# Kernel optimization log

Measured on AMD Instinct MI355X. Metric: run time of the kernel, lower is better.

The kernel has to match this reference:

```python
import jax, jax.numpy as jnp
import numpy as np

K = 20
EPS = 1e-5


def _bn(h, g, b, axes):
    m = jnp.mean(h, axes, keepdims=True)
    v = jnp.var(h, axes, keepdims=True)
    return (h - m) * jax.lax.rsqrt(v + EPS) * g + b


def _edge_feat(h):
    # h: [B,N,D] -> edge features [B,N,K,2D] = concat(central, neighbor-central)
    sq = jnp.sum(h * h, -1)
    # negative squared pairwise distance (larger = closer)
    adj = 2.0 * jnp.einsum('bnd,bmd->bnm', h, h) - sq[:, :, None] - sq[:, None, :]
    idx = jax.lax.top_k(adj, K)[1]  # [B,N,K] nearest (incl. self)
    nbr = jax.vmap(lambda hb, ib: hb[ib])(h, idx)  # [B,N,K,D]
    ctr = jnp.broadcast_to(h[:, :, None, :], nbr.shape)
    return jnp.concatenate([ctr, nbr - ctr], -1)


def _edge_layer(h, W, b, g, be):
    # 1x1 conv over edge features, relu THEN batchnorm (matches torch: bn(relu(conv))), max over K
    ef = _edge_feat(h)
    z = jax.nn.relu(jnp.einsum('bnkc,oc->bnko', ef, W) + b)
    z = _bn(z, g, be, (0, 1, 2))
    return jnp.max(z, axis=2)  # [B,N,O]


def _c1d(h, W, b):
    return jnp.einsum('bcl,oc->bol', h, W) + b[None, :, None]


def _bnc(h, g, b):
    m = jnp.mean(h, (0, 2), keepdims=True)
    v = jnp.var(h, (0, 2), keepdims=True)
    return (h - m) * jax.lax.rsqrt(v + EPS) * g[None, :, None] + b[None, :, None]


def _forward(x, rand_grid, W1, b1, g1, be1, W2, b2, g2, be2, W3, b3, g3, be3,
             W4, b4, g4, be4, W5, b5, g5, be5, lW, lb, lg, lbe,
             dW1, db1, dg1, dbe1, dW2, db2, dg2, dbe2, dW3, db3, dg3, dbe3, dW4, db4):
    pts = jnp.transpose(x, (0, 2, 1))  # [B,N,3]
    x1 = _edge_layer(pts, W1, b1, g1, be1)   # [B,N,64]
    x2 = _edge_layer(x1, W2, b2, g2, be2)    # [B,N,64]
    x3 = _edge_layer(x2, W3, b3, g3, be3)    # [B,N,64]
    x4 = _edge_layer(x3, W4, b4, g4, be4)    # [B,N,128]
    cat = jnp.concatenate([x1, x2, x3, x4], -1)  # [B,N,320]
    z = jax.nn.relu(jnp.einsum('bnc,oc->bno', cat, W5) + b5)
    z = _bn(z, g5, be5, (0, 1))
    glob = jnp.max(z, axis=1)  # [B,1024]
    lat = glob @ lW.T + lb
    lat = jax.nn.relu(_bn(lat, lg, lbe, (0,)))  # [B,1024]
    B, C = lat.shape
    P = rand_grid.shape[2]
    y = jnp.concatenate([rand_grid, jnp.broadcast_to(lat[:, :, None], (B, C, P))], axis=1)  # [B,1026,P]
    h = jax.nn.relu(_bnc(_c1d(y, dW1, db1), dg1, dbe1))
    h = jax.nn.relu(_bnc(_c1d(h, dW2, db2), dg2, dbe2))
    h = jax.nn.relu(_bnc(_c1d(h, dW3, db3), dg3, dbe3))
    return jnp.tanh(_c1d(h, dW4, db4))  # [B,3,P]


def setup_inputs() -> dict:
    key = jax.random.key(0)
    ks = iter(jax.random.split(key, 64))
    B, N, BOT = 8, 2048, 1024
    D = BOT + 2  # 1026
    f32 = jnp.float32

    def w(o, c):
        return jax.random.normal(next(ks), (o, c), dtype=f32) * 0.05

    def bnp(c):
        return jnp.ones((c,), f32), jnp.zeros((c,), f32)

    inp = {
        'x': jax.random.normal(next(ks), (B, 3, N), dtype=f32),
        'rand_grid': jax.random.uniform(next(ks), (B, 2, N), dtype=f32),
    }
    enc = [(64, 6), (64, 128), (64, 128), (128, 128), (1024, 320)]
    for i, (o, c) in enumerate(enc, 1):
        inp[f'W{i}'] = w(o, c)
        inp[f'b{i}'] = jnp.zeros((o,), f32)
        inp[f'g{i}'], inp[f'be{i}'] = bnp(o)
    inp['lW'] = w(BOT, 1024)
    inp['lb'] = jnp.zeros((BOT,), f32)
    inp['lg'], inp['lbe'] = bnp(BOT)
    dec = [(D, D), (D // 2, D), (D // 4, D // 2), (3, D // 4)]
    for i, (o, c) in enumerate(dec, 1):
        inp[f'dW{i}'] = w(o, c)
        inp[f'db{i}'] = jnp.zeros((o,), f32)
        if i < 4:
            inp[f'dg{i}'], inp[f'dbe{i}'] = bnp(o)
    return inp


def reference(x, rand_grid, W1, b1, g1, be1, W2, b2, g2, be2, W3, b3, g3, be3,
              W4, b4, g4, be4, W5, b5, g5, be5, lW, lb, lg, lbe,
              dW1, db1, dg1, dbe1, dW2, db2, dg2, dbe2, dW3, db3, dg3, dbe3, dW4, db4):
    return _forward(x, rand_grid, W1, b1, g1, be1, W2, b2, g2, be2, W3, b3, g3, be3,
                    W4, b4, g4, be4, W5, b5, g5, be5, lW, lb, lg, lbe,
                    dW1, db1, dg1, dbe1, dW2, db2, dg2, dbe2, dW3, db3, dg3, dbe3, dW4, db4)
```

## Files before the change

### kernel.cpp

```cpp
#include <hip/hip_runtime.h>
#include <math.h>

constexpr int NB = 8;
constexpr int NN = 2048;
constexpr int NK = 20;
constexpr int NP = 2048;


__global__ void transpose_x_kernel(const float* __restrict__ x, float* __restrict__ pts) {
  int gid = blockIdx.x * 256 + threadIdx.x;
  if (gid >= NB * NN * 3) return;
  int c = gid % 3;
  int n = (gid / 3) % NN;
  int b = gid / (3 * NN);
  pts[gid] = x[(b * 3 + c) * NN + n];
}

__global__ void transpose_mat_ld(const float* __restrict__ src, float* __restrict__ dst, int R,
                                 int C, int ldd) {
  __shared__ float tile[32][33];
  int c0 = blockIdx.x * 32, r0 = blockIdx.y * 32;
  int tx = threadIdx.x & 31, ty = threadIdx.x >> 5;
  for (int i = ty; i < 32; i += 8) {
    int r = r0 + i, c = c0 + tx;
    tile[i][tx] = (r < R && c < C) ? src[(size_t)r * C + c] : 0.f;
  }
  __syncthreads();
  for (int i = ty; i < 32; i += 8) {
    int c = c0 + i, r = r0 + tx;
    if (r < R && c < C) dst[(size_t)c * ldd + r] = tile[tx][i];
  }
}

__global__ void knn3_fused_kernel(const float* __restrict__ pts, int* __restrict__ idx) {
  __shared__ float sm[3][NN];
  int t = threadIdx.x;
  int l = t & 63, w = t >> 6;
  int gb = blockIdx.x;
  int b = gb >> 9;
  int n0 = (gb & 511) * 4;
  const float* base = pts + (size_t)b * NN * 3;
  for (int e = t; e < NN * 3; e += 256) {
    int col = e / 3, d = e - col * 3;
    sm[d][col] = base[e];
  }
  __syncthreads();
  int n = n0 + w;
  float c0 = sm[0][n], c1 = sm[1][n], c2 = sm[2][n];
  float v[32];
#pragma unroll
  for (int j = 0; j < 32; j++) {
    int col = j * 64 + l;
    float d0 = c0 - sm[0][col];
    float d1 = c1 - sm[1][col];
    float d2 = c2 - sm[2][col];
    float acc = 0.f;
    acc = fmaf(d0, d0, acc);
    acc = fmaf(d1, d1, acc);
    acc = fmaf(d2, d2, acc);
    v[j] = -acc;
  }
  int mykm = 0;
  for (int k = 0; k < NK; k++) {
    float bv = v[0];
    int bj = 0;
#pragma unroll
    for (int j = 1; j < 32; j++) {
      if (v[j] > bv) { bv = v[j]; bj = j; }
    }
    int gm = bj * 64 + l;
#pragma unroll
    for (int off = 32; off; off >>= 1) {
      float ov = __shfl_xor(bv, off, 64);
      int om = __shfl_xor(gm, off, 64);
      if (ov > bv || (ov == bv && om < gm)) { bv = ov; gm = om; }
    }
    if (l == k) mykm = gm;
    int jb = gm >> 6, lb = gm & 63;
#pragma unroll
    for (int j = 0; j < 32; j++)
      if (j == jb && l == lb) v[j] = -3e38f;
  }
  if (l < NK) idx[((size_t)(b * NN + n)) * NK + l] = mykm;
}

__global__ __launch_bounds__(1024) void knn64_fused_kernel(const float* __restrict__ h, int ld,
                                                           int coff, int* __restrict__ idx) {
  __shared__ float sft[64][128];
  __shared__ float sctr[16][64];
  int t = threadIdx.x;
  int l = t & 63, w = t >> 6;
  int n0 = blockIdx.x * 16;
  int b = blockIdx.y;
  const float* rows = h + (size_t)b * NN * ld + coff;
  {
    int r = t >> 6, d = t & 63;
    sctr[r][d] = rows[(size_t)(n0 + r) * ld + d];
  }
  int col_l = t >> 3;
  int d0 = (t & 7) * 8;
  float v[32];
#pragma unroll
  for (int ct = 0; ct < 16; ct++) {
    __syncthreads();
    {
      const float* src = &rows[(size_t)(ct * 128 + col_l) * ld + d0];
      float4 f0 = *(const float4*)src;
      float4 f1 = *(const float4*)(src + 4);
      sft[d0 + 0][col_l] = f0.x;
      sft[d0 + 1][col_l] = f0.y;
      sft[d0 + 2][col_l] = f0.z;
      sft[d0 + 3][col_l] = f0.w;
      sft[d0 + 4][col_l] = f1.x;
      sft[d0 + 5][col_l] = f1.y;
      sft[d0 + 6][col_l] = f1.z;
      sft[d0 + 7][col_l] = f1.w;
    }
    __syncthreads();
    float a0 = 0.f, a1 = 0.f;
#pragma unroll 8
    for (int d = 0; d < 64; d++) {
      float cd = sctr[w][d];
      float2 f = *(const float2*)&sft[d][2 * l];
      float e0 = cd - f.x, e1 = cd - f.y;
      a0 = fmaf(e0, e0, a0);
      a1 = fmaf(e1, e1, a1);
    }
    v[2 * ct] = -a0;
    v[2 * ct + 1] = -a1;
  }
  int mykm = 0;
  for (int k = 0; k < NK; k++) {
    float bv = v[0];
    int bj = 0;
#pragma unroll
    for (int j = 1; j < 32; j++) {
      if (v[j] > bv) { bv = v[j]; bj = j; }
    }
    int gm = ((bj >> 1) << 7) + 2 * l + (bj & 1);
#pragma unroll
    for (int off = 32; off; off >>= 1) {
      float ov = __shfl_xor(bv, off, 64);
      int om = __shfl_xor(gm, off, 64);
      if (ov > bv || (ov == bv && om < gm)) { bv = ov; gm = om; }
    }
    if (l == k) mykm = gm;
    int rem = gm & 127;
    int jb = ((gm >> 7) << 1) + (rem & 1);
    int lb = rem >> 1;
#pragma unroll
    for (int j = 0; j < 32; j++)
      if (j == jb && l == lb) v[j] = -3e38f;
  }
  if (l < NK) idx[((size_t)(b * NN + n0 + w)) * NK + l] = mykm;
}

__global__ void weff_kernel(const float* __restrict__ W, int O, int D, float* __restrict__ Weff) {
  int i = blockIdx.x * 256 + threadIdx.x;
  if (i >= 2 * O * D) return;
  int o = i / D, d = i - o * D;
  float v;
  if (o < O) v = W[(size_t)o * 2 * D + d] - W[(size_t)o * 2 * D + D + d];
  else v = W[(size_t)(o - O) * 2 * D + D + d];
  Weff[i] = v;
}

template <int M2, int D>
__global__ __launch_bounds__(256, 4) void pgemm_kernel(const float* __restrict__ h, int ld,
                                                       int coff, const float* __restrict__ Weff,
                                                       const float* __restrict__ bias,
                                                       float* __restrict__ P) {
  constexpr int O = M2 / 2;
  constexpr int GRP = 256 / M2;
  constexpr int NR = 8 / GRP;
  __shared__ float sh[8][D == 3 ? 4 : 68];
  int t = threadIdx.x;
  int n0 = blockIdx.x * 8;
  const float* base = h + coff;
  if constexpr (D == 64) {
    if (t < 128) {
      int r = t >> 4, q = (t & 15) * 4;
      *(float4*)&sh[r][q] = *(const float4*)&base[(size_t)(n0 + r) * ld + q];
    }
  } else {
    if (t < 24) {
      int r = t / 3, c = t - r * 3;
      sh[r][c] = base[(size_t)(n0 + r) * ld + c];
    }
  }
  __syncthreads();
  int o = t % M2;
  int gi = t / M2;
  float acc[NR];
  float bz = (o < O) ? bias[o] : 0.f;
#pragma unroll
  for (int j = 0; j < NR; j++) acc[j] = bz;
  const float* wr = Weff + (size_t)o * D;
  if constexpr (D == 64) {
#pragma unroll
    for (int d4 = 0; d4 < 16; d4++) {
      float4 w4 = *(const float4*)&wr[d4 * 4];
#pragma unroll
      for (int j = 0; j < NR; j++) {
        float4 e4 = *(const float4*)&sh[gi * NR + j][d4 * 4];
        acc[j] = fmaf(w4.x, e4.x, acc[j]);
        acc[j] = fmaf(w4.y, e4.y, acc[j]);
        acc[j] = fmaf(w4.z, e4.z, acc[j]);
        acc[j] = fmaf(w4.w, e4.w, acc[j]);
      }
    }
  } else {
    float w0 = wr[0], w1 = wr[1], w2 = wr[2];
#pragma unroll
    for (int j = 0; j < NR; j++) {
      int r = gi * NR + j;
      acc[j] = fmaf(w0, sh[r][0], fmaf(w1, sh[r][1], fmaf(w2, sh[r][2], acc[j])));
    }
  }
#pragma unroll
  for (int j = 0; j < NR; j++)
    P[(size_t)(n0 + gi * NR + j) * M2 + o] = acc[j];
}

template <int O>
__global__ __launch_bounds__(256, 8) void combine_kernel(const float* __restrict__ P,
                                                         const int* __restrict__ idx,
                                                         float* __restrict__ zmax,
                                                         float* __restrict__ zmin,
                                                         float* __restrict__ psum,
                                                         float* __restrict__ psq) {
  constexpr int CPB = 256 / O;
  constexpr int M2 = 2 * O;
  __shared__ int sidx[CPB * NK];
  int t = threadIdx.x;
  int bn0 = blockIdx.x * CPB;
  if (t < CPB * NK) sidx[t] = idx[(size_t)bn0 * NK + t];
  __syncthreads();
  int g = t / O, o = t % O;
  int bn = bn0 + g;
  int b = bn >> 11;
  float p1 = P[(size_t)bn * M2 + o];
  const float* P2 = P + (size_t)b * NN * M2 + O + o;
  float s = 0.f, sq = 0.f, mx = -3e38f, mn = 3e38f;
#pragma unroll
  for (int k = 0; k < NK; k++) {
    int nb = sidx[g * NK + k];
    float z = fmaxf(p1 + P2[(size_t)nb * M2], 0.f);
    s += z;
    sq = fmaf(z, z, sq);
    mx = fmaxf(mx, z);
    mn = fminf(mn, z);
  }
  zmax[(size_t)bn * O + o] = mx;
  zmin[(size_t)bn * O + o] = mn;
  psum[(size_t)o * (NB * NN) + bn] = s;
  psq[(size_t)o * (NB * NN) + bn] = sq;
}

__global__ void edge_reduce_kernel(const float* __restrict__ psum, const float* __restrict__ psq,
                                   const float* __restrict__ g, const float* __restrict__ be,
                                   float* __restrict__ scale, float* __restrict__ shift,
                                   double inv_n) {
  int o = blockIdx.x, t = threadIdx.x;
  double s = 0.0, q = 0.0;
  const float* ps = psum + (size_t)o * (NB * NN);
  const float* pq = psq + (size_t)o * (NB * NN);
  for (int i = t; i < NB * NN; i += 256) { s += (double)ps[i]; q += (double)pq[i]; }
  __shared__ double rs[256], rq[256];
  rs[t] = s; rq[t] = q;
  __syncthreads();
  for (int st = 128; st; st >>= 1) {
    if (t < st) { rs[t] += rs[t + st]; rq[t] += rq[t + st]; }
    __syncthreads();
  }
  if (t == 0) {
    double mean = rs[0] * inv_n;
    double var = rq[0] * inv_n - mean * mean;
    double r = 1.0 / sqrt(var + 1e-5);
    double sc = (double)g[o] * r;
    scale[o] = (float)sc;
    shift[o] = (float)((double)be[o] - mean * sc);
  }
}

__global__ void edge_affine_kernel(const float* __restrict__ zmax, const float* __restrict__ zmin,
                                   const float* __restrict__ scale, const float* __restrict__ shift,
                                   float* __restrict__ cat, int O, int coff_out) {
  int gid = blockIdx.x * 256 + threadIdx.x;
  int o = gid % O;
  int bn = gid / O;
  float sc = scale[o];
  float v = (sc >= 0.f) ? zmax[gid] : zmin[gid];
  cat[(size_t)bn * 320 + coff_out + o] = fmaf(sc, v, shift[o]);
}

__global__ __launch_bounds__(256, 2) void gemm5_64_kernel(const float* __restrict__ cat,
                                                          const float* __restrict__ W5t,
                                                          const float* __restrict__ b5,
                                                          float* __restrict__ z5) {
  __shared__ float sA[32][64];
  __shared__ float sB[32][128];
  int t = threadIdx.x;
  int r0 = blockIdx.x * 64, m0 = blockIdx.y * 128;
  int arow = t & 63, ach = (t >> 6) * 8;
  int blr = t >> 4, blc = (t & 15) * 8;
  int tx = t & 15, ty = t >> 4;
  float acc[4][8] = {};
  float rA[8], rB[16];

  auto gload = [&](int c0) {
    const float* pa = &cat[(size_t)(r0 + arow) * 320 + c0 + ach];
    float4 a0 = *(const float4*)pa;
    float4 a1 = *(const float4*)(pa + 4);
    rA[0] = a0.x; rA[1] = a0.y; rA[2] = a0.z; rA[3] = a0.w;
    rA[4] = a1.x; rA[5] = a1.y; rA[6] = a1.z; rA[7] = a1.w;
    const float* pb = &W5t[(size_t)(c0 + blr) * 1024 + m0 + blc];
    float4 b0 = *(const float4*)pb;
    float4 b1 = *(const float4*)(pb + 4);
    rB[0] = b0.x; rB[1] = b0.y; rB[2] = b0.z; rB[3] = b0.w;
    rB[4] = b1.x; rB[5] = b1.y; rB[6] = b1.z; rB[7] = b1.w;
    const float* pb2 = &W5t[(size_t)(c0 + 16 + blr) * 1024 + m0 + blc];
    float4 c4 = *(const float4*)pb2;
    float4 c5 = *(const float4*)(pb2 + 4);
    rB[8] = c4.x; rB[9] = c4.y; rB[10] = c4.z; rB[11] = c4.w;
    rB[12] = c5.x; rB[13] = c5.y; rB[14] = c5.z; rB[15] = c5.w;
  };
  auto ldswrite = [&]() {
#pragma unroll
    for (int j = 0; j < 8; j++) sA[ach + j][arow] = rA[j];
    float4 w0, w1;
    w0.x = rB[0]; w0.y = rB[1]; w0.z = rB[2]; w0.w = rB[3];
    w1.x = rB[4]; w1.y = rB[5]; w1.z = rB[6]; w1.w = rB[7];
    *(float4*)&sB[blr][blc] = w0;
    *(float4*)&sB[blr][blc + 4] = w1;
    w0.x = rB[8]; w0.y = rB[9]; w0.z = rB[10]; w0.w = rB[11];
    w1.x = rB[12]; w1.y = rB[13]; w1.z = rB[14]; w1.w = rB[15];
    *(float4*)&sB[16 + blr][blc] = w0;
    *(float4*)&sB[16 + blr][blc + 4] = w1;
  };

  gload(0);
  for (int kt = 0; kt < 10; kt++) {
    __syncthreads();
    ldswrite();
    __syncthreads();
    if (kt + 1 < 10) gload((kt + 1) * 32);
#pragma unroll
    for (int c = 0; c < 32; c++) {
      float4 a0 = *(const float4*)&sA[c][ty * 4];
      float4 b0 = *(const float4*)&sB[c][tx * 4];
      float4 b1 = *(const float4*)&sB[c][64 + tx * 4];
      float av[4] = {a0.x, a0.y, a0.z, a0.w};
      float bv[8] = {b0.x, b0.y, b0.z, b0.w, b1.x, b1.y, b1.z, b1.w};
#pragma unroll
      for (int i = 0; i < 4; i++)
#pragma unroll
        for (int j = 0; j < 8; j++) acc[i][j] = fmaf(av[i], bv[j], acc[i][j]);
    }
  }
  float bj[8];
#pragma unroll
  for (int j = 0; j < 8; j++)
    bj[j] = b5[m0 + (j < 4 ? tx * 4 + j : 64 + tx * 4 + (j - 4))];
#pragma unroll
  for (int i = 0; i < 4; i++) {
    int r = r0 + ty * 4 + i;
    float* dst = &z5[(size_t)r * 1024 + m0];
    float4 q0, q1;
    q0.x = fmaxf(acc[i][0] + bj[0], 0.f);
    q0.y = fmaxf(acc[i][1] + bj[1], 0.f);
    q0.z = fmaxf(acc[i][2] + bj[2], 0.f);
    q0.w = fmaxf(acc[i][3] + bj[3], 0.f);
    q1.x = fmaxf(acc[i][4] + bj[4], 0.f);
    q1.y = fmaxf(acc[i][5] + bj[5], 0.f);
    q1.z = fmaxf(acc[i][6] + bj[6], 0.f);
    q1.w = fmaxf(acc[i][7] + bj[7], 0.f);
    *(float4*)&dst[tx * 4] = q0;
    *(float4*)&dst[64 + tx * 4] = q1;
  }
}

__global__ void stats5_kernel(const float* __restrict__ z5, double* __restrict__ psum5,
                              double* __restrict__ psq5, float* __restrict__ pmax5,
                              float* __restrict__ pmin5) {
  int j = blockIdx.x, t = threadIdx.x;
  int row0 = j * 64;
  double s0 = 0, s1 = 0, s2 = 0, s3 = 0, q0 = 0, q1 = 0, q2 = 0, q3 = 0;
  float4 mx = {-3e38f, -3e38f, -3e38f, -3e38f}, mn = {3e38f, 3e38f, 3e38f, 3e38f};
  for (int r = 0; r < 64; r++) {
    float4 v = *(const float4*)&z5[(size_t)(row0 + r) * 1024 + t * 4];
    s0 += v.x; s1 += v.y; s2 += v.z; s3 += v.w;
    q0 += (double)v.x * v.x; q1 += (double)v.y * v.y;
    q2 += (double)v.z * v.z; q3 += (double)v.w * v.w;
    mx.x = fmaxf(mx.x, v.x); mx.y = fmaxf(mx.y, v.y); mx.z = fmaxf(mx.z, v.z); mx.w = fmaxf(mx.w, v.w);
    mn.x = fminf(mn.x, v.x); mn.y = fminf(mn.y, v.y); mn.z = fminf(mn.z, v.z); mn.w = fminf(mn.w, v.w);
  }
  size_t base = (size_t)j * 1024 + t * 4;
  psum5[base + 0] = s0; psum5[base + 1] = s1; psum5[base + 2] = s2; psum5[base + 3] = s3;
  psq5[base + 0] = q0; psq5[base + 1] = q1; psq5[base + 2] = q2; psq5[base + 3] = q3;
  *(float4*)&pmax5[base] = mx;
  *(float4*)&pmin5[base] = mn;
}

__global__ void reduce5_glob_kernel(const double* __restrict__ psum5, const double* __restrict__ psq5,
                                    const float* __restrict__ pmax5, const float* __restrict__ pmin5,
                                    const float* __restrict__ g5, const float* __restrict__ be5,
                                    float* __restrict__ glob) {
  int o = blockIdx.x * 256 + threadIdx.x;
  double s = 0.0, q = 0.0;
  for (int j = 0; j < 256; j++) {
    s += psum5[(size_t)j * 1024 + o];
    q += psq5[(size_t)j * 1024 + o];
  }
  double mean = s * (1.0 / 16384.0);
  double var = q * (1.0 / 16384.0) - mean * mean;
  double r = 1.0 / sqrt(var + 1e-5);
  double scd = (double)g5[o] * r;
  float sc = (float)scd;
  float sh = (float)((double)be5[o] - mean * scd);
  for (int b = 0; b < 8; b++) {
    float m;
    if (sc >= 0.f) {
      m = -3e38f;
      for (int jj = 0; jj < 32; jj++) m = fmaxf(m, pmax5[(size_t)(b * 32 + jj) * 1024 + o]);
    } else {
      m = 3e38f;
      for (int jj = 0; jj < 32; jj++) m = fminf(m, pmin5[(size_t)(b * 32 + jj) * 1024 + o]);
    }
    glob[b * 1024 + o] = fmaf(sc, m, sh);
  }
}

__global__ void fc_kernel(const float* __restrict__ in, const float* __restrict__ Wt, int ld,
                          int coff, const float* __restrict__ bias, float* __restrict__ out,
                          int Ci, int Co) {
  __shared__ float sin_[1024];
  __shared__ float red[8][32];
  int b = blockIdx.x, t = threadIdx.x;
  for (int e = t; e < Ci; e += 256) sin_[e] = in[(size_t)b * Ci + e];
  __syncthreads();
  int o = blockIdx.y * 32 + (t & 31);
  int cg = t >> 5;
  int cn = Ci / 8;
  float p = 0.f;
  if (o < Co) {
    for (int c = cg * cn; c < (cg + 1) * cn; c++)
      p = fmaf(Wt[(size_t)(c + coff) * ld + o], sin_[c], p);
  }
  red[cg][t & 31] = p;
  __syncthreads();
  if (cg == 0 && o < Co) {
    float s = red[0][t] + red[1][t] + red[2][t] + red[3][t] + red[4][t] + red[5][t] + red[6][t] +
              red[7][t];
    out[(size_t)b * Co + o] = s + bias[o];
  }
}

__global__ void lat_bn_kernel(const float* __restrict__ latp, const float* __restrict__ lg,
                              const float* __restrict__ lbe, float* __restrict__ lat) {
  int o = blockIdx.x * 256 + threadIdx.x;
  float v[8];
  double s = 0.0, q = 0.0;
  for (int b = 0; b < 8; b++) {
    v[b] = latp[b * 1024 + o];
    s += (double)v[b];
    q += (double)v[b] * (double)v[b];
  }
  double mean = s * 0.125;
  double var = q * 0.125 - mean * mean;
  double r = 1.0 / sqrt(var + 1e-5);
  double gd = (double)lg[o], bd = (double)lbe[o];
  for (int b = 0; b < 8; b++) {
    float z = (float)(((double)v[b] - mean) * r * gd + bd);
    lat[b * 1024 + o] = fmaxf(z, 0.f);
  }
}

__global__ void dec1_z_kernel(const float* __restrict__ rg, const float* __restrict__ dW1t,
                              const float* __restrict__ u, float* __restrict__ z1) {
  int bo = blockIdx.x;
  int b = bo / 1026;
  int o = bo - b * 1026;
  int t = threadIdx.x;
  float w0 = dW1t[o], w1 = dW1t[1026 + o], ub = u[bo];
  const float4* r0 = (const float4*)(rg + (size_t)b * 2 * NP);
  const float4* r1 = (const float4*)(rg + (size_t)b * 2 * NP + NP);
  float4* zr = (float4*)(z1 + (size_t)bo * NP);
  for (int i = t; i < NP / 4; i += 256) {
    float4 a = r0[i], c = r1[i], rr;
    rr.x = fmaf(w0, a.x, fmaf(w1, c.x, ub));
    rr.y = fmaf(w0, a.y, fmaf(w1, c.y, ub));
    rr.z = fmaf(w0, a.z, fmaf(w1, c.z, ub));
    rr.w = fmaf(w0, a.w, fmaf(w1, c.w, ub));
    zr[i] = rr;
  }
}

__global__ void dstats_kernel(const float* __restrict__ z, int C, const float* __restrict__ g,
                              const float* __restrict__ be, float* __restrict__ scale,
                              float* __restrict__ shift) {
  int o = blockIdx.x, t = threadIdx.x;
  double s = 0.0, q = 0.0;
  for (int b = 0; b < 8; b++) {
    const float4* row = (const float4*)(z + ((size_t)b * C + o) * NP);
    for (int i = t; i < NP / 4; i += 256) {
      float4 v = row[i];
      s += (double)v.x + (double)v.y + (double)v.z + (double)v.w;
      q += (double)v.x * v.x + (double)v.y * v.y + (double)v.z * v.z + (double)v.w * v.w;
    }
  }
  __shared__ double rs[256], rq[256];
  rs[t] = s; rq[t] = q;
  __syncthreads();
  for (int st = 128; st; st >>= 1) {
    if (t < st) { rs[t] += rs[t + st]; rq[t] += rq[t + st]; }
    __syncthreads();
  }
  if (t == 0) {
    double inv = 1.0 / (8.0 * NP);
    double mean = rs[0] * inv;
    double var = rq[0] * inv - mean * mean;
    double r = 1.0 / sqrt(var + 1e-5);
    double sc = (double)g[o] * r;
    scale[o] = (float)sc;
    shift[o] = (float)((double)be[o] - mean * sc);
  }
}

template <int NMT>
__global__ __launch_bounds__(256, 2) void dec_gemm64s_kernel(
    const float* __restrict__ zin, const float* __restrict__ Wt, int ldA,
    const float* __restrict__ bias, const float* __restrict__ scale,
    const float* __restrict__ shift, float* __restrict__ zout, int Ci, int Co) {
  __shared__ float sA[32][64];
  __shared__ float sB[32][128];
  int bid = blockIdx.x;
  int gl = bid & 7;
  int q = bid >> 3;
  int gh = q / NMT;
  int mt = q - gh * NMT;
  int g = gl + (gh << 3);
  int pt = g & 15;
  int b = g >> 4;
  int m0 = mt * 64, p0 = pt * 128;
  int t = threadIdx.x;
  int lr = t >> 4, lcA = (t & 15) * 4, lcB = (t & 15) * 8;
  int tx = t & 15, ty = t >> 4;
  int numK = (Ci + 31) >> 5;
  float acc[4][8] = {};
  float rA[8], rB[16];

  auto gloadhalf = [&](int c, float* ra, float* rb) {
#pragma unroll
    for (int j = 0; j < 4; j++) ra[j] = 0.f;
#pragma unroll
    for (int j = 0; j < 8; j++) rb[j] = 0.f;
    if (c < Ci) {
      int mb = m0 + lcA;
      if (mb + 4 <= Co) {
        float4 a0 = *(const float4*)&Wt[(size_t)c * ldA + mb];
        ra[0] = a0.x; ra[1] = a0.y; ra[2] = a0.z; ra[3] = a0.w;
      } else {
#pragma unroll
        for (int j = 0; j < 4; j++)
          if (mb + j < Co) ra[j] = Wt[(size_t)c * ldA + mb + j];
      }
      float sc = scale[c], sh = shift[c];
      const float* src = &zin[((size_t)b * Ci + c) * NP + p0 + lcB];
      float4 z0 = *(const float4*)src;
      float4 z1 = *(const float4*)(src + 4);
      rb[0] = fmaxf(fmaf(sc, z0.x, sh), 0.f);
      rb[1] = fmaxf(fmaf(sc, z0.y, sh), 0.f);
      rb[2] = fmaxf(fmaf(sc, z0.z, sh), 0.f);
      rb[3] = fmaxf(fmaf(sc, z0.w, sh), 0.f);
      rb[4] = fmaxf(fmaf(sc, z1.x, sh), 0.f);
      rb[5] = fmaxf(fmaf(sc, z1.y, sh), 0.f);
      rb[6] = fmaxf(fmaf(sc, z1.z, sh), 0.f);
      rb[7] = fmaxf(fmaf(sc, z1.w, sh), 0.f);
    }
  };
  auto gload = [&](int kt) {
    gloadhalf(kt * 32 + lr, rA, rB);
    gloadhalf(kt * 32 + 16 + lr, rA + 4, rB + 8);
  };
  auto ldswrite = [&]() {
    float4 v0;
    v0.x = rA[0]; v0.y = rA[1]; v0.z = rA[2]; v0.w = rA[3];
    *(float4*)&sA[lr][lcA] = v0;
    v0.x = rA[4]; v0.y = rA[5]; v0.z = rA[6]; v0.w = rA[7];
    *(float4*)&sA[16 + lr][lcA] = v0;
    float4 w0, w1;
    w0.x = rB[0]; w0.y = rB[1]; w0.z = rB[2]; w0.w = rB[3];
    w1.x = rB[4]; w1.y = rB[5]; w1.z = rB[6]; w1.w = rB[7];
    *(float4*)&sB[lr][lcB] = w0;
    *(float4*)&sB[lr][lcB + 4] = w1;
    w0.x = rB[8]; w0.y = rB[9]; w0.z = rB[10]; w0.w = rB[11];
    w1.x = rB[12]; w1.y = rB[13]; w1.z = rB[14]; w1.w = rB[15];
    *(float4*)&sB[16 + lr][lcB] = w0;
    *(float4*)&sB[16 + lr][lcB + 4] = w1;
  };

  gload(0);
  for (int kt = 0; kt < numK; kt++) {
    __syncthreads();
    ldswrite();
    __syncthreads();
    if (kt + 1 < numK) gload(kt + 1);
#pragma unroll
    for (int c = 0; c < 32; c++) {
      float4 a0 = *(const float4*)&sA[c][ty * 4];
      float4 b0 = *(const float4*)&sB[c][tx * 4];
      float4 b1 = *(const float4*)&sB[c][64 + tx * 4];
      float av[4] = {a0.x, a0.y, a0.z, a0.w};
      float bv[8] = {b0.x, b0.y, b0.z, b0.w, b1.x, b1.y, b1.z, b1.w};
#pragma unroll
      for (int i = 0; i < 4; i++)
#pragma unroll
        for (int j = 0; j < 8; j++) acc[i][j] = fmaf(av[i], bv[j], acc[i][j]);
    }
  }
#pragma unroll
  for (int i = 0; i < 4; i++) {
    int m = m0 + ty * 4 + i;
    if (m < Co) {
      float bv = bias[m];
      float* dst = &zout[((size_t)b * Co + m) * NP + p0];
      float4 q0, q1;
      q0.x = acc[i][0] + bv; q0.y = acc[i][1] + bv;
      q0.z = acc[i][2] + bv; q0.w = acc[i][3] + bv;
      q1.x = acc[i][4] + bv; q1.y = acc[i][5] + bv;
      q1.z = acc[i][6] + bv; q1.w = acc[i][7] + bv;
      *(float4*)&dst[tx * 4] = q0;
      *(float4*)&dst[64 + tx * 4] = q1;
    }
  }
}

__global__ void dec_final_kernel(const float* __restrict__ z3, const float* __restrict__ dW4,
                                 const float* __restrict__ db4, const float* __restrict__ scale,
                                 const float* __restrict__ shift, float* __restrict__ out) {
  __shared__ float w4[3 * 256];
  __shared__ float sc[256], sh[256];
  __shared__ float red[4][64][3];
  int b = blockIdx.x, pc = blockIdx.y, t = threadIdx.x;
  for (int e = t; e < 768; e += 256) w4[e] = dW4[e];
  sc[t] = scale[t];
  sh[t] = shift[t];
  __syncthreads();
  int tp = t & 63, tc = t >> 6;
  int p = pc * 64 + tp;
  float a0 = 0.f, a1 = 0.f, a2 = 0.f;
  for (int c = tc * 64; c < tc * 64 + 64; c++) {
    float hv = fmaxf(fmaf(sc[c], z3[((size_t)(b * 256 + c)) * NP + p], sh[c]), 0.f);
    a0 = fmaf(w4[c], hv, a0);
    a1 = fmaf(w4[256 + c], hv, a1);
    a2 = fmaf(w4[512 + c], hv, a2);
  }
  red[tc][tp][0] = a0;
  red[tc][tp][1] = a1;
  red[tc][tp][2] = a2;
  __syncthreads();
  if (tc == 0) {
    a0 = red[0][tp][0] + red[1][tp][0] + red[2][tp][0] + red[3][tp][0];
    a1 = red[0][tp][1] + red[1][tp][1] + red[2][tp][1] + red[3][tp][1];
    a2 = red[0][tp][2] + red[1][tp][2] + red[2][tp][2] + red[3][tp][2];
    out[((size_t)b * 3 + 0) * NP + p] = tanhf(a0 + db4[0]);
    out[((size_t)b * 3 + 1) * NP + p] = tanhf(a1 + db4[1]);
    out[((size_t)b * 3 + 2) * NP + p] = tanhf(a2 + db4[2]);
  }
}


extern "C" void kernel_launch(void* const* d_in, const int* in_sizes, int n_in, void* d_out,
                              int out_size, void* d_ws, size_t ws_size, hipStream_t stream) {
  const float* x = (const float*)d_in[0];
  const float* rg = (const float*)d_in[1];
  const float* W1 = (const float*)d_in[2];
  const float* b1 = (const float*)d_in[3];
  const float* g1 = (const float*)d_in[4];
  const float* be1 = (const float*)d_in[5];
  const float* W2 = (const float*)d_in[6];
  const float* b2 = (const float*)d_in[7];
  const float* g2 = (const float*)d_in[8];
  const float* be2 = (const float*)d_in[9];
  const float* W3 = (const float*)d_in[10];
  const float* b3 = (const float*)d_in[11];
  const float* g3 = (const float*)d_in[12];
  const float* be3 = (const float*)d_in[13];
  const float* W4 = (const float*)d_in[14];
  const float* b4 = (const float*)d_in[15];
  const float* g4 = (const float*)d_in[16];
  const float* be4 = (const float*)d_in[17];
  const float* W5 = (const float*)d_in[18];
  const float* b5 = (const float*)d_in[19];
  const float* g5 = (const float*)d_in[20];
  const float* be5 = (const float*)d_in[21];
  const float* lW = (const float*)d_in[22];
  const float* lb = (const float*)d_in[23];
  const float* lg = (const float*)d_in[24];
  const float* lbe = (const float*)d_in[25];
  const float* dW1 = (const float*)d_in[26];
  const float* db1 = (const float*)d_in[27];
  const float* dg1 = (const float*)d_in[28];
  const float* dbe1 = (const float*)d_in[29];
  const float* dW2 = (const float*)d_in[30];
  const float* db2 = (const float*)d_in[31];
  const float* dg2 = (const float*)d_in[32];
  const float* dbe2 = (const float*)d_in[33];
  const float* dW3 = (const float*)d_in[34];
  const float* db3 = (const float*)d_in[35];
  const float* dg3 = (const float*)d_in[36];
  const float* dbe3 = (const float*)d_in[37];
  const float* dW4 = (const float*)d_in[38];
  const float* db4 = (const float*)d_in[39];
  float* out = (float*)d_out;

  float* ws = (float*)d_ws;
  size_t off = 0;
  auto alloc = [&](size_t n) {
    size_t r = off;
    off += (n + 255) & ~(size_t)255;
    return r;
  };
  size_t f_pts = alloc((size_t)NB * NN * 3);
  size_t f_uA = alloc(13959168);
  size_t f_cat = f_uA;
  size_t f_idx = f_cat + 5242880;
  size_t f_zmax = f_idx + 327680;
  size_t f_zmin = f_zmax + 2097152;
  size_t f_psum = f_zmin + 2097152;
  size_t f_psq = f_psum + 2097152;
  size_t f_z2 = f_uA;
  size_t f_uB = alloc(16809984);
  size_t f_z5 = f_uB, f_z1 = f_uB;
  float* P = ws + f_uB;
  size_t f_uC = alloc(4194304);
  double* ps5_d = (double*)(ws + f_uC);
  double* pq5_d = ps5_d + 262144;
  size_t f_pM5 = f_uC + 2097152;
  size_t f_pm5 = f_pM5 + 262144;
  size_t f_z3 = f_uC;
  size_t f_weff = alloc(256 * 64);
  size_t f_W5t = alloc(320 * 1024);
  size_t f_lWt = alloc(1024 * 1024);
  size_t f_dW1t = alloc((size_t)1026 * 1026);
  size_t f_dW2t = alloc((size_t)1026 * 516);
  size_t f_dW3t = alloc(513 * 256);
  size_t f_scale = alloc(2048);
  size_t f_shift = alloc(2048);
  size_t f_glob = alloc(8 * 1024);
  size_t f_latp = alloc(8 * 1024);
  size_t f_lat = alloc(8 * 1024);
  size_t f_u = alloc(8 * 1026);
  (void)ws_size;
  (void)in_sizes;
  (void)n_in;
  (void)out_size;

  float* cat = ws + f_cat;
  int* idxp = (int*)(ws + f_idx);
  float* zmax = ws + f_zmax;
  float* zmin = ws + f_zmin;
  float* psumf = ws + f_psum;
  float* psqf = ws + f_psq;
  float* weff = ws + f_weff;
  float* scale = ws + f_scale;
  float* shift = ws + f_shift;
  const double invn_e = 1.0 / (double)(NB * NN * NK);

  transpose_x_kernel<<<192, 256, 0, stream>>>(x, ws + f_pts);
  transpose_mat_ld<<<dim3(10, 32), 256, 0, stream>>>(W5, ws + f_W5t, 1024, 320, 1024);
  transpose_mat_ld<<<dim3(32, 32), 256, 0, stream>>>(lW, ws + f_lWt, 1024, 1024, 1024);
  transpose_mat_ld<<<dim3(33, 33), 256, 0, stream>>>(dW1, ws + f_dW1t, 1026, 1026, 1026);
  transpose_mat_ld<<<dim3(33, 17), 256, 0, stream>>>(dW2, ws + f_dW2t, 513, 1026, 516);
  transpose_mat_ld<<<dim3(17, 8), 256, 0, stream>>>(dW3, ws + f_dW3t, 256, 513, 256);

  knn3_fused_kernel<<<NB * NN / 4, 256, 0, stream>>>(ws + f_pts, idxp);
  weff_kernel<<<2, 256, 0, stream>>>(W1, 64, 3, weff);
  pgemm_kernel<128, 3><<<2048, 256, 0, stream>>>(ws + f_pts, 3, 0, weff, b1, P);
  combine_kernel<64><<<4096, 256, 0, stream>>>(P, idxp, zmax, zmin, psumf, psqf);
  edge_reduce_kernel<<<64, 256, 0, stream>>>(psumf, psqf, g1, be1, scale, shift, invn_e);
  edge_affine_kernel<<<NB * NN * 64 / 256, 256, 0, stream>>>(zmax, zmin, scale, shift, cat, 64, 0);
  knn64_fused_kernel<<<dim3(128, 8), 1024, 0, stream>>>(cat, 320, 0, idxp);
  weff_kernel<<<32, 256, 0, stream>>>(W2, 64, 64, weff);
  pgemm_kernel<128, 64><<<2048, 256, 0, stream>>>(cat, 320, 0, weff, b2, P);
  combine_kernel<64><<<4096, 256, 0, stream>>>(P, idxp, zmax, zmin, psumf, psqf);
  edge_reduce_kernel<<<64, 256, 0, stream>>>(psumf, psqf, g2, be2, scale, shift, invn_e);
  edge_affine_kernel<<<NB * NN * 64 / 256, 256, 0, stream>>>(zmax, zmin, scale, shift, cat, 64, 64);
  knn64_fused_kernel<<<dim3(128, 8), 1024, 0, stream>>>(cat, 320, 64, idxp);
  weff_kernel<<<32, 256, 0, stream>>>(W3, 64, 64, weff);
  pgemm_kernel<128, 64><<<2048, 256, 0, stream>>>(cat, 320, 64, weff, b3, P);
  combine_kernel<64><<<4096, 256, 0, stream>>>(P, idxp, zmax, zmin, psumf, psqf);
  edge_reduce_kernel<<<64, 256, 0, stream>>>(psumf, psqf, g3, be3, scale, shift, invn_e);
  edge_affine_kernel<<<NB * NN * 64 / 256, 256, 0, stream>>>(zmax, zmin, scale, shift, cat, 64, 128);
  knn64_fused_kernel<<<dim3(128, 8), 1024, 0, stream>>>(cat, 320, 128, idxp);
  weff_kernel<<<64, 256, 0, stream>>>(W4, 128, 64, weff);
  pgemm_kernel<256, 64><<<2048, 256, 0, stream>>>(cat, 320, 128, weff, b4, P);
  combine_kernel<128><<<8192, 256, 0, stream>>>(P, idxp, zmax, zmin, psumf, psqf);
  edge_reduce_kernel<<<128, 256, 0, stream>>>(psumf, psqf, g4, be4, scale, shift, invn_e);
  edge_affine_kernel<<<NB * NN * 128 / 256, 256, 0, stream>>>(zmax, zmin, scale, shift, cat, 128, 192);

  gemm5_64_kernel<<<dim3(256, 8), 256, 0, stream>>>(cat, ws + f_W5t, b5, ws + f_z5);
  stats5_kernel<<<256, 256, 0, stream>>>(ws + f_z5, ps5_d, pq5_d, ws + f_pM5, ws + f_pm5);
  reduce5_glob_kernel<<<4, 256, 0, stream>>>(ps5_d, pq5_d, ws + f_pM5, ws + f_pm5, g5, be5,
                                             ws + f_glob);
  fc_kernel<<<dim3(8, 32), 256, 0, stream>>>(ws + f_glob, ws + f_lWt, 1024, 0, lb, ws + f_latp,
                                             1024, 1024);
  lat_bn_kernel<<<4, 256, 0, stream>>>(ws + f_latp, lg, lbe, ws + f_lat);
  fc_kernel<<<dim3(8, 33), 256, 0, stream>>>(ws + f_lat, ws + f_dW1t, 1026, 2, db1, ws + f_u, 1024,
                                             1026);
  dec1_z_kernel<<<8 * 1026, 256, 0, stream>>>(rg, ws + f_dW1t, ws + f_u, ws + f_z1);
  dstats_kernel<<<1026, 256, 0, stream>>>(ws + f_z1, 1026, dg1, dbe1, scale, shift);
  dec_gemm64s_kernel<9><<<9 * 128, 256, 0, stream>>>(ws + f_z1, ws + f_dW2t, 516, db2, scale,
                                                     shift, ws + f_z2, 1026, 513);
  dstats_kernel<<<513, 256, 0, stream>>>(ws + f_z2, 513, dg2, dbe2, scale, shift);
  dec_gemm64s_kernel<4><<<4 * 128, 256, 0, stream>>>(ws + f_z2, ws + f_dW3t, 256, db3, scale,
                                                     shift, ws + f_z3, 513, 256);
  dstats_kernel<<<256, 256, 0, stream>>>(ws + f_z3, 256, dg3, dbe3, scale, shift);
  dec_final_kernel<<<dim3(8, 32), 256, 0, stream>>>(ws + f_z3, dW4, db4, scale, shift, out);
}
```

Measured before the change: 1.908 ms.

## Register-block knn64 so each wave computes distances for four query points

The 64-dim kNN kernel now runs with 256 threads per block, and each wave handles four query points instead of one. Every candidate feature loaded from shared memory is reused across the four queries, which cuts LDS traffic per FMA, and the tile fill uses wider per-thread loads. The cost is four 32-entry distance arrays held in registers per thread, which raises register pressure and lowers the number of resident waves. The top-k selection now runs serially four times per wave.

Measured after the change: 2.019 ms. 1.06x slower.

```diff
diff --git a/kernel.cpp b/kernel.cpp
--- a/kernel.cpp
+++ b/kernel.cpp
@@ -84,8 +84,8 @@
   if (l < NK) idx[((size_t)(b * NN + n)) * NK + l] = mykm;
 }
 
-__global__ __launch_bounds__(1024) void knn64_fused_kernel(const float* __restrict__ h, int ld,
-                                                           int coff, int* __restrict__ idx) {
+__global__ __launch_bounds__(256, 2) void knn64_fused4_kernel(const float* __restrict__ h, int ld,
+                                                              int coff, int* __restrict__ idx) {
   __shared__ float sft[64][128];
   __shared__ float sctr[16][64];
   int t = threadIdx.x;
@@ -93,66 +93,79 @@
   int n0 = blockIdx.x * 16;
   int b = blockIdx.y;
   const float* rows = h + (size_t)b * NN * ld + coff;
-  {
-    int r = t >> 6, d = t & 63;
+  for (int e = t; e < 16 * 64; e += 256) {
+    int r = e >> 6, d = e & 63;
     sctr[r][d] = rows[(size_t)(n0 + r) * ld + d];
   }
-  int col_l = t >> 3;
-  int d0 = (t & 7) * 8;
-  float v[32];
+  int colg = t & 127;
+  int dh = (t >> 7) * 32;
+  float v[4][32];
 #pragma unroll
   for (int ct = 0; ct < 16; ct++) {
     __syncthreads();
     {
-      const float* src = &rows[(size_t)(ct * 128 + col_l) * ld + d0];
-      float4 f0 = *(const float4*)src;
-      float4 f1 = *(const float4*)(src + 4);
-      sft[d0 + 0][col_l] = f0.x;
-      sft[d0 + 1][col_l] = f0.y;
-      sft[d0 + 2][col_l] = f0.z;
-      sft[d0 + 3][col_l] = f0.w;
-      sft[d0 + 4][col_l] = f1.x;
-      sft[d0 + 5][col_l] = f1.y;
-      sft[d0 + 6][col_l] = f1.z;
-      sft[d0 + 7][col_l] = f1.w;
+      const float* src = &rows[(size_t)(ct * 128 + colg) * ld + dh];
+#pragma unroll
+      for (int q = 0; q < 8; q++) {
+        float4 f = *(const float4*)(src + q * 4);
+        sft[dh + q * 4 + 0][colg] = f.x;
+        sft[dh + q * 4 + 1][colg] = f.y;
+        sft[dh + q * 4 + 2][colg] = f.z;
+        sft[dh + q * 4 + 3][colg] = f.w;
+      }
     }
     __syncthreads();
-    float a0 = 0.f, a1 = 0.f;
+    float a00 = 0.f, a01 = 0.f, a10 = 0.f, a11 = 0.f;
+    float a20 = 0.f, a21 = 0.f, a30 = 0.f, a31 = 0.f;
 #pragma unroll 8
     for (int d = 0; d < 64; d++) {
-      float cd = sctr[w][d];
-      float2 f = *(const float2*)&sft[d][2 * l];
-      float e0 = cd - f.x, e1 = cd - f.y;
-      a0 = fmaf(e0, e0, a0);
-      a1 = fmaf(e1, e1, a1);
-    }
-    v[2 * ct] = -a0;
-    v[2 * ct + 1] = -a1;
-  }
-  int mykm = 0;
-  for (int k = 0; k < NK; k++) {
-    float bv = v[0];
-    int bj = 0;
-#pragma unroll
-    for (int j = 1; j < 32; j++) {
-      if (v[j] > bv) { bv = v[j]; bj = j; }
-    }
-    int gm = ((bj >> 1) << 7) + 2 * l + (bj & 1);
-#pragma unroll
-    for (int off = 32; off; off >>= 1) {
-      float ov = __shfl_xor(bv, off, 64);
-      int om = __shfl_xor(gm, off, 64);
-      if (ov > bv || (ov == bv && om < gm)) { bv = ov; gm = om; }
-    }
-    if (l == k) mykm = gm;
-    int rem = gm & 127;
-    int jb = ((gm >> 7) << 1) + (rem & 1);
-    int lb = rem >> 1;
-#pragma unroll
-    for (int j = 0; j < 32; j++)
-      if (j == jb && l == lb) v[j] = -3e38f;
-  }
-  if (l < NK) idx[((size_t)(b * NN + n0 + w)) * NK + l] = mykm;
+      float f0 = sft[d][l];
+      float f1 = sft[d][64 + l];
+      float c0v = sctr[4 * w + 0][d];
+      float c1v = sctr[4 * w + 1][d];
+      float c2v = sctr[4 * w + 2][d];
+      float c3v = sctr[4 * w + 3][d];
+      float e;
+      e = c0v - f0; a00 = fmaf(e, e, a00);
+      e = c0v - f1; a01 = fmaf(e, e, a01);
+      e = c1v - f0; a10 = fmaf(e, e, a10);
+      e = c1v - f1; a11 = fmaf(e, e, a11);
+      e = c2v - f0; a20 = fmaf(e, e, a20);
+      e = c2v - f1; a21 = fmaf(e, e, a21);
+      e = c3v - f0; a30 = fmaf(e, e, a30);
+      e = c3v - f1; a31 = fmaf(e, e, a31);
+    }
+    v[0][2 * ct] = -a00; v[0][2 * ct + 1] = -a01;
+    v[1][2 * ct] = -a10; v[1][2 * ct + 1] = -a11;
+    v[2][2 * ct] = -a20; v[2][2 * ct + 1] = -a21;
+    v[3][2 * ct] = -a30; v[3][2 * ct + 1] = -a31;
+  }
+#pragma unroll
+  for (int ci = 0; ci < 4; ci++) {
+    int mykm = 0;
+    for (int k = 0; k < NK; k++) {
+      float bv = v[ci][0];
+      int bj = 0;
+#pragma unroll
+      for (int j = 1; j < 32; j++) {
+        if (v[ci][j] > bv) { bv = v[ci][j]; bj = j; }
+      }
+      int gm = ((bj >> 1) << 7) + ((bj & 1) << 6) + l;
+#pragma unroll
+      for (int off = 32; off; off >>= 1) {
+        float ov = __shfl_xor(bv, off, 64);
+        int om = __shfl_xor(gm, off, 64);
+        if (ov > bv || (ov == bv && om < gm)) { bv = ov; gm = om; }
+      }
+      if (l == k) mykm = gm;
+      int jb = ((gm >> 7) << 1) + ((gm >> 6) & 1);
+      int lb = gm & 63;
+#pragma unroll
+      for (int j = 0; j < 32; j++)
+        if (j == jb && l == lb) v[ci][j] = -3e38f;
+    }
+    if (l < NK) idx[((size_t)(b * NN + n0 + 4 * w + ci)) * NK + l] = mykm;
+  }
 }
 
 __global__ void weff_kernel(const float* __restrict__ W, int O, int D, float* __restrict__ Weff) {
@@ -781,19 +794,19 @@
   combine_kernel<64><<<4096, 256, 0, stream>>>(P, idxp, zmax, zmin, psumf, psqf);
   edge_reduce_kernel<<<64, 256, 0, stream>>>(psumf, psqf, g1, be1, scale, shift, invn_e);
   edge_affine_kernel<<<NB * NN * 64 / 256, 256, 0, stream>>>(zmax, zmin, scale, shift, cat, 64, 0);
-  knn64_fused_kernel<<<dim3(128, 8), 1024, 0, stream>>>(cat, 320, 0, idxp);
+  knn64_fused4_kernel<<<dim3(128, 8), 256, 0, stream>>>(cat, 320, 0, idxp);
   weff_kernel<<<32, 256, 0, stream>>>(W2, 64, 64, weff);
   pgemm_kernel<128, 64><<<2048, 256, 0, stream>>>(cat, 320, 0, weff, b2, P);
   combine_kernel<64><<<4096, 256, 0, stream>>>(P, idxp, zmax, zmin, psumf, psqf);
   edge_reduce_kernel<<<64, 256, 0, stream>>>(psumf, psqf, g2, be2, scale, shift, invn_e);
   edge_affine_kernel<<<NB * NN * 64 / 256, 256, 0, stream>>>(zmax, zmin, scale, shift, cat, 64, 64);
-  knn64_fused_kernel<<<dim3(128, 8), 1024, 0, stream>>>(cat, 320, 64, idxp);
+  knn64_fused4_kernel<<<dim3(128, 8), 256, 0, stream>>>(cat, 320, 64, idxp);
   weff_kernel<<<32, 256, 0, stream>>>(W3, 64, 64, weff);
   pgemm_kernel<128, 64><<<2048, 256, 0, stream>>>(cat, 320, 64, weff, b3, P);
   combine_kernel<64><<<4096, 256, 0, stream>>>(P, idxp, zmax, zmin, psumf, psqf);
   edge_reduce_kernel<<<64, 256, 0, stream>>>(psumf, psqf, g3, be3, scale, shift, invn_e);
   edge_affine_kernel<<<NB * NN * 64 / 256, 256, 0, stream>>>(zmax, zmin, scale, shift, cat, 64, 128);
-  knn64_fused_kernel<<<dim3(128, 8), 1024, 0, stream>>>(cat, 320, 128, idxp);
+  knn64_fused4_kernel<<<dim3(128, 8), 256, 0, stream>>>(cat, 320, 128, idxp);
   weff_kernel<<<64, 256, 0, stream>>>(W4, 128, 64, weff);
   pgemm_kernel<256, 64><<<2048, 256, 0, stream>>>(cat, 320, 128, weff, b4, P);
   combine_kernel<128><<<8192, 256, 0, stream>>>(P, idxp, zmax, zmin, psumf, psqf);
```
